# Performance work log

Measured on AMD Instinct MI355X. Metric: run time of the kernel, lower is better.

Reference implementation:

```python
import jax, jax.numpy as jnp
import numpy as np

B, T, N, F = 32, 64, 256, 64
TOP_K = 0.2  # ratio of dims to keep per batch element


def setup_inputs() -> dict:
    key = jax.random.key(0)
    ks = jax.random.split(key, 12)
    w = lambda k, shape: jax.random.normal(k, shape, jnp.float32) * 0.05
    z = lambda: jnp.zeros((F,), jnp.float32)
    return {
        "x": jax.random.normal(ks[0], (B, T, N, F), jnp.float32),
        "Wc1": w(ks[1], (3, F, F)), "bc1": z(),
        "Wc2": w(ks[2], (3, F, F)), "bc2": z(),
        "Wc3": w(ks[3], (3, F, F)), "bc3": z(),
        "Wq": w(ks[4], (F, F)), "bq": z(),
        "Wk": w(ks[5], (F, F)), "bk": z(),
        "Wv": w(ks[6], (F, F)), "bv": z(),
        "Wd": w(ks[7], (F, F)), "bd": z(),
        "Wp": w(ks[8], (F, F)), "bp": z(),
    }


def _conv1d(x, W, b, dil):
    # x: [BN, T, F], W: [3, F, F] (WIO), dilated same-padded conv over time
    y = jax.lax.conv_general_dilated(
        x, W, window_strides=(1,), padding="SAME", rhs_dilation=(dil,),
        dimension_numbers=("NWC", "WIO", "NWC"))
    return y + b


@jax.custom_vjp
def ste_round(x):
    return jnp.round(x)

def _ste_fwd(x):
    return jnp.round(x), None

def _ste_bwd(res, g):
    # activation='linear': grad = upstream * 1
    return (g,)

ste_round.defvjp(_ste_fwd, _ste_bwd)


def reference(x, Wc1, bc1, Wc2, bc2, Wc3, bc3, Wq, bq, Wk, bk, Wv, bv, Wd, bd, Wp, bp):
    Bx, Tx, Nx, Fx = x.shape
    # --- dilated conv block over time axis (per node) ---
    xt = jnp.transpose(x, (0, 2, 1, 3)).reshape(Bx * Nx, Tx, Fx)  # [BN,T,F]
    c = jax.nn.relu(_conv1d(xt, Wc1, bc1, 1) + _conv1d(xt, Wc2, bc2, 2)
                    + _conv1d(xt, Wc3, bc3, 3))
    xt = xt + c
    x = jnp.transpose(xt.reshape(Bx, Nx, Tx, Fx), (0, 2, 1, 3))  # [B,T,N,F]
    # --- GAT attention over nodes (faithful: diagonal einsum 'btnn,btnf->btnf') ---
    Q = x @ Wq + bq
    K = x @ Wk + bk
    V = x @ Wv + bv
    scores = jnp.einsum("btnf,btmf->btnm", Q, K) / jnp.sqrt(jnp.float32(Fx))
    A = jax.nn.softmax(scores, axis=-1)
    g = jnp.einsum("btnn,btnf->btnf", A, V)  # diag(A) * V, as in the TF source
    x = x + jax.nn.relu(g)
    # --- dense projection ---
    x = x @ Wd + bd
    # --- inf-norm normalize over last axis, rescale to [0,1] ---
    norm = jnp.max(jnp.abs(x), axis=-1, keepdims=True)
    x = x / norm
    x = 0.5 * (x + 1.0)
    # --- per-batch top-k threshold via full sort ---
    n = Tx * Nx * Fx
    k = int(round(TOP_K * n))  # top_k < 1 => ratio, statically resolved
    ranking = jnp.sort(x.reshape(Bx, -1), axis=-1)  # ascending
    mu = ranking[:, -k - 1].reshape(Bx, 1, 1, 1)
    x = jax.nn.sigmoid(x - mu)
    # --- straight-through binary mask + frozen linear predictor ---
    mask = ste_round(x)
    masked = x * mask
    pred_on_masked = masked @ Wp + bp
    return pred_on_masked, mask
```

## Files before the change

kernel.cpp:

```cpp
#include <hip/hip_runtime.h>
#include <math.h>

#define BB 32
#define TT 64
#define NNODES 256
#define FDIM 64
#define SLICE (NNODES*FDIM)
#define NTOT (BB*TT*NNODES*FDIM)
#define RANK0 838860u

typedef float v2f __attribute__((ext_vector_type(2)));
__device__ __forceinline__ v2f pkfma(v2f a, v2f b, v2f c) {
#if __has_builtin(__builtin_elementwise_fma)
  return __builtin_elementwise_fma(a, b, c);
#else
  v2f r; r.x = fmaf(a.x,b.x,c.x); r.y = fmaf(a.y,b.y,c.y); return r;
#endif
}

__global__ __launch_bounds__(256) void combine_w(
    const float* __restrict__ Wc1, const float* __restrict__ bc1,
    const float* __restrict__ Wc2, const float* __restrict__ bc2,
    const float* __restrict__ Wc3, const float* __restrict__ bc3,
    float* __restrict__ Wcomb, float* __restrict__ bcomb)
{
  const int FF2 = FDIM*FDIM;
  int gid = blockIdx.x*256 + threadIdx.x;
  if (gid < 7*FF2) {
    int j = gid / FF2, r = gid % FF2;
    float v;
    switch (j) {
      case 0: v = Wc3[r]; break;
      case 1: v = Wc2[r]; break;
      case 2: v = Wc1[r]; break;
      case 3: v = Wc1[FF2+r] + Wc2[FF2+r] + Wc3[FF2+r]; break;
      case 4: v = Wc1[2*FF2+r]; break;
      case 5: v = Wc2[2*FF2+r]; break;
      default: v = Wc3[2*FF2+r]; break;
    }
    Wcomb[gid] = v;
  }
  if (gid < FDIM) bcomb[gid] = bc1[gid] + bc2[gid] + bc3[gid];
}

__global__ __launch_bounds__(256) void combine_qk(
    const float* __restrict__ Wq, const float* __restrict__ bq,
    const float* __restrict__ Wk, const float* __restrict__ bk,
    float* __restrict__ Wqk, float* __restrict__ zb,
    float* __restrict__ wqbk, float* __restrict__ bqbk)
{
  int gid = blockIdx.x*256 + threadIdx.x;
  if (gid < 4096) {
    int i = gid >> 6, j = gid & 63;
    float a = 0.f;
    for (int o=0;o<64;o++) a = fmaf(Wq[i*64+o], Wk[j*64+o], a);
    Wqk[i*64+j] = a;
  } else if (gid < 4160) {
    int j = gid - 4096;
    float a = 0.f;
    for (int o=0;o<64;o++) a = fmaf(bq[o], Wk[j*64+o], a);
    zb[j] = a;
  } else if (gid < 4224) {
    int i = gid - 4160;
    float a = 0.f;
    for (int o=0;o<64;o++) a = fmaf(Wq[i*64+o], bk[o], a);
    wqbk[i] = a;
  } else if (gid == 4224) {
    float a = 0.f;
    for (int o=0;o<64;o++) a = fmaf(bq[o], bk[o], a);
    bqbk[0] = a;
  }
}

__global__ __launch_bounds__(256,4) void conv_kernel(
    const float* __restrict__ x, const float* __restrict__ Wcomb,
    const float* __restrict__ bcomb, float* __restrict__ x1)
{
  __shared__ float xs[64*72];
  const int bn = blockIdx.x; const int b = bn >> 8; const int n = bn & 255;
  const int tid = threadIdx.x;
#pragma unroll
  for (int k=0;k<18;k++) xs[k*256+tid] = 0.f;
  __syncthreads();
  const float* xbase = x + ((size_t)b*TT)*SLICE + n*FDIM;
#pragma unroll
  for (int it=0; it<4; it++) {
    int flat4 = it*256 + tid;
    int t = flat4 >> 4, f4 = (flat4 & 15) << 2;
    float4 v = *(const float4*)(xbase + (size_t)t*SLICE + f4);
    xs[(f4+0)*72 + t+4] = v.x;
    xs[(f4+1)*72 + t+4] = v.y;
    xs[(f4+2)*72 + t+4] = v.z;
    xs[(f4+3)*72 + t+4] = v.w;
  }
  __syncthreads();
  const int o = tid & 63;
  const int tb = (tid >> 6) << 4;
  float acc[16];
  const float bco = bcomb[o];
#pragma unroll
  for (int k=0;k<16;k++) acc[k] = bco;
  for (int i=0;i<FDIM;i++) {
    float xr[24];
#pragma unroll
    for (int q=0;q<6;q++) {
      float4 v = *(const float4*)&xs[i*72 + tb + q*4];
      xr[q*4+0]=v.x; xr[q*4+1]=v.y; xr[q*4+2]=v.z; xr[q*4+3]=v.w;
    }
#pragma unroll
    for (int j=0;j<7;j++) {
      float w = Wcomb[(j*FDIM+i)*FDIM + o];
#pragma unroll
      for (int k=0;k<16;k++) acc[k] = fmaf(xr[k+j+1], w, acc[k]);
    }
  }
  float* obase = x1 + ((size_t)b*TT)*SLICE + n*FDIM + o;
#pragma unroll
  for (int k=0;k<16;k++) {
    int t = tb + k;
    float c = acc[k];
    float outv = xs[o*72 + t+4] + (c > 0.f ? c : 0.f);
    obase[(size_t)t*SLICE] = outv;
  }
}

__global__ __launch_bounds__(256,2) void attn_kernel(
    const float* __restrict__ x1,
    const float* __restrict__ Wqk, const float* __restrict__ zb,
    const float* __restrict__ wqbk, const float* __restrict__ bqbk,
    const float* __restrict__ Wv, const float* __restrict__ bv,
    const float* __restrict__ Wd, const float* __restrict__ bd,
    float* __restrict__ vout)
{
  __shared__ float ks[NNODES*68];
  const int bt = blockIdx.x;
  const int tid = threadIdx.x;
  const float4* xb4 = (const float4*)(x1 + (size_t)bt*SLICE);
#pragma unroll
  for (int it=0; it<16; it++) {
    int flat4 = it*256 + tid;
    int n = flat4 >> 4, f4 = (flat4 & 15) << 2;
    *(float4*)&ks[n*68 + f4] = xb4[flat4];
  }
  __syncthreads();

  v2f zp[32];
  float d = bqbk[0];
  {
    float xr[64];
#pragma unroll
    for (int q=0;q<16;q++) {
      float4 v = *(const float4*)&ks[tid*68 + q*4];
      xr[q*4+0]=v.x; xr[q*4+1]=v.y; xr[q*4+2]=v.z; xr[q*4+3]=v.w;
    }
#pragma unroll
    for (int j=0;j<32;j++) { v2f t; t.x = zb[2*j]; t.y = zb[2*j+1]; zp[j] = t; }
    for (int i=0;i<64;i++) {
      v2f xv; xv.x = xr[i]; xv.y = xr[i];
      const float4* wr = (const float4*)(Wqk + i*64);
#pragma unroll
      for (int q=0;q<16;q++) {
        float4 w4 = wr[q];
        v2f wlo; wlo.x=w4.x; wlo.y=w4.y;
        v2f whi; whi.x=w4.z; whi.y=w4.w;
        zp[2*q]   = pkfma(xv, wlo, zp[2*q]);
        zp[2*q+1] = pkfma(xv, whi, zp[2*q+1]);
      }
      d = fmaf(xr[i], wqbk[i], d);
    }
  }

  float S0 = 0.f, S1 = 0.f, diag = 0.f;
  for (int m=0;m<NNODES;m+=2) {
    v2f a0={0.f,0.f}, a1={0.f,0.f}, b0={0.f,0.f}, b1={0.f,0.f};
#pragma unroll
    for (int q=0;q<16;q++) {
      float4 k0 = *(const float4*)&ks[m*68 + q*4];
      float4 k1 = *(const float4*)&ks[(m+1)*68 + q*4];
      v2f k0lo; k0lo.x=k0.x; k0lo.y=k0.y;
      v2f k0hi; k0hi.x=k0.z; k0hi.y=k0.w;
      v2f k1lo; k1lo.x=k1.x; k1lo.y=k1.y;
      v2f k1hi; k1hi.x=k1.z; k1hi.y=k1.w;
      a0 = pkfma(zp[2*q],   k0lo, a0);
      a1 = pkfma(zp[2*q+1], k0hi, a1);
      b0 = pkfma(zp[2*q],   k1lo, b0);
      b1 = pkfma(zp[2*q+1], k1hi, b1);
    }
    float s0 = (((a0.x+a0.y)+(a1.x+a1.y)) + d)*0.125f;
    float s1 = (((b0.x+b0.y)+(b1.x+b1.y)) + d)*0.125f;
    if (tid == m)   diag = s0;
    if (tid == m+1) diag = s1;
    S0 += __expf(s0);
    S1 += __expf(s1);
  }
  const float ann = __expf(diag) / (S0 + S1);

  float o1[64];
  {
    float xr[64];
#pragma unroll
    for (int q=0;q<16;q++) {
      float4 v = *(const float4*)&ks[tid*68 + q*4];
      xr[q*4+0]=v.x; xr[q*4+1]=v.y; xr[q*4+2]=v.z; xr[q*4+3]=v.w;
    }
    v2f vacc[32];
#pragma unroll
    for (int j=0;j<32;j++) { v2f t; t.x = bv[2*j]; t.y = bv[2*j+1]; vacc[j] = t; }
    for (int i=0;i<64;i++) {
      v2f xv; xv.x = xr[i]; xv.y = xr[i];
      const float4* wr = (const float4*)(Wv + i*64);
#pragma unroll
      for (int q=0;q<16;q++) {
        float4 w4 = wr[q];
        v2f wlo; wlo.x=w4.x; wlo.y=w4.y;
        v2f whi; whi.x=w4.z; whi.y=w4.w;
        vacc[2*q]   = pkfma(xv, wlo, vacc[2*q]);
        vacc[2*q+1] = pkfma(xv, whi, vacc[2*q+1]);
      }
    }
#pragma unroll
    for (int o=0;o<64;o++) {
      float g = ann * ((o & 1) ? vacc[o>>1].y : vacc[o>>1].x);
      o1[o] = xr[o] + (g > 0.f ? g : 0.f);
    }
  }
  float dd[64];
  {
    v2f dacc[32];
#pragma unroll
    for (int j=0;j<32;j++) { v2f t; t.x = bd[2*j]; t.y = bd[2*j+1]; dacc[j] = t; }
    for (int i=0;i<64;i++) {
      v2f xv; xv.x = o1[i]; xv.y = o1[i];
      const float4* wr = (const float4*)(Wd + i*64);
#pragma unroll
      for (int q=0;q<16;q++) {
        float4 w4 = wr[q];
        v2f wlo; wlo.x=w4.x; wlo.y=w4.y;
        v2f whi; whi.x=w4.z; whi.y=w4.w;
        dacc[2*q]   = pkfma(xv, wlo, dacc[2*q]);
        dacc[2*q+1] = pkfma(xv, whi, dacc[2*q+1]);
      }
    }
#pragma unroll
    for (int o=0;o<64;o++) dd[o] = (o & 1) ? dacc[o>>1].y : dacc[o>>1].x;
  }
  float nrm = 0.f;
#pragma unroll
  for (int o=0;o<64;o++) nrm = fmaxf(nrm, fabsf(dd[o]));
  __syncthreads();
#pragma unroll
  for (int q=0;q<16;q++) {
    float4 w;
    w.x = 0.5f*(dd[q*4+0]/nrm + 1.f);
    w.y = 0.5f*(dd[q*4+1]/nrm + 1.f);
    w.z = 0.5f*(dd[q*4+2]/nrm + 1.f);
    w.w = 0.5f*(dd[q*4+3]/nrm + 1.f);
    *(float4*)&ks[tid*68 + q*4] = w;
  }
  __syncthreads();
  float4* ob4 = (float4*)(vout + (size_t)bt*SLICE);
#pragma unroll
  for (int it=0;it<16;it++) {
    int flat4 = it*256 + tid;
    int n = flat4 >> 4, f4 = (flat4 & 15) << 2;
    ob4[flat4] = *(const float4*)&ks[n*68 + f4];
  }
}

template<int LEVEL>
__global__ __launch_bounds__(256) void hist_kernel(
    const float* __restrict__ v, unsigned* __restrict__ ghist,
    const unsigned* __restrict__ pfx)
{
  __shared__ unsigned h[4096];
  const int batch = blockIdx.x >> 5, chunk = blockIdx.x & 31;
  const int tid = threadIdx.x;
#pragma unroll
  for (int k=0;k<16;k++) h[k*256+tid] = 0u;
  __syncthreads();
  const unsigned p = pfx ? pfx[batch] : 0u;
  const float4* vb = (const float4*)(v + (size_t)batch*(TT*SLICE)) + chunk*8192 + tid;
  for (int k=0;k<32;k++) {
    float4 q = vb[k*256];
    float e[4] = {q.x,q.y,q.z,q.w};
#pragma unroll
    for (int j=0;j<4;j++) {
      unsigned u = __float_as_uint(e[j]);
      if (LEVEL==1) atomicAdd(&h[u>>20], 1u);
      else if ((u>>20)==p) atomicAdd(&h[(u>>8)&0xFFFu], 1u);
    }
  }
  __syncthreads();
  unsigned* gh = ghist + batch*4096;
#pragma unroll
  for (int k=0;k<16;k++) { unsigned c = h[k*256+tid]; if (c) atomicAdd(&gh[k*256+tid], c); }
}

__global__ __launch_bounds__(256) void hist8_kernel(
    const float* __restrict__ v, unsigned* __restrict__ ghist,
    const unsigned* __restrict__ pfx)
{
  __shared__ unsigned h[256];
  const int batch = blockIdx.x >> 5, chunk = blockIdx.x & 31;
  const int tid = threadIdx.x;
  h[tid] = 0u;
  __syncthreads();
  const unsigned p = pfx[batch];
  const float4* vb = (const float4*)(v + (size_t)batch*(TT*SLICE)) + chunk*8192 + tid;
  for (int k=0;k<32;k++) {
    float4 q = vb[k*256];
    float e[4] = {q.x,q.y,q.z,q.w};
#pragma unroll
    for (int j=0;j<4;j++) {
      unsigned u = __float_as_uint(e[j]);
      if ((u>>8)==p) atomicAdd(&h[u & 255u], 1u);
    }
  }
  __syncthreads();
  unsigned c = h[tid];
  if (c) atomicAdd(&ghist[batch*256+tid], c);
}

template<int PER>
__global__ __launch_bounds__(256) void find_kernel(
    const unsigned* __restrict__ hist,
    const unsigned* __restrict__ rank_in, const unsigned* __restrict__ pfx_in,
    int pfx_shift, unsigned* __restrict__ pfx_out, unsigned* __restrict__ rank_out,
    float* __restrict__ mu, int final_level)
{
  __shared__ unsigned csum[256];
  const int batch = blockIdx.x;
  const int tid = threadIdx.x;
  const unsigned* hb = hist + batch*(PER*256);
  unsigned loc[PER];
  unsigned s = 0;
#pragma unroll
  for (int q=0;q<PER;q++) { loc[q] = hb[tid*PER+q]; s += loc[q]; }
  csum[tid] = s;
  __syncthreads();
  for (int off=1; off<256; off<<=1) {
    unsigned vv = csum[tid];
    unsigned ad = (tid >= off) ? csum[tid-off] : 0u;
    __syncthreads();
    csum[tid] = vv + ad;
    __syncthreads();
  }
  const unsigned rank = rank_in ? rank_in[batch] : RANK0;
  const unsigned excl = csum[tid] - s;
  if (rank >= excl && rank < excl + s) {
    unsigned r = rank - excl;
    int bin = 0;
#pragma unroll
    for (int q=0;q<PER;q++) {
      if (r < loc[q]) { bin = tid*PER + q; break; }
      r -= loc[q];
    }
    unsigned pf = pfx_in ? pfx_in[batch] : 0u;
    unsigned np = (pf << pfx_shift) | (unsigned)bin;
    if (final_level) { mu[batch] = __uint_as_float(np); }
    else { pfx_out[batch] = np; rank_out[batch] = r; }
  }
}

__global__ __launch_bounds__(256,2) void final_kernel(
    const float* __restrict__ v, const float* __restrict__ mu,
    const float* __restrict__ Wp, const float* __restrict__ bp,
    float* __restrict__ pred, float* __restrict__ mask)
{
  __shared__ float sl[NNODES*68];
  const int bt = blockIdx.x;
  const int b = bt >> 6;
  const int tid = threadIdx.x;
  const float4* vb4 = (const float4*)(v + (size_t)bt*SLICE);
#pragma unroll
  for (int it=0; it<16; it++) {
    int flat4 = it*256 + tid;
    int n = flat4 >> 4, f4 = (flat4 & 15) << 2;
    *(float4*)&sl[n*68 + f4] = vb4[flat4];
  }
  __syncthreads();
  const float muv = mu[b];
  float srow[64];
#pragma unroll
  for (int q=0;q<16;q++) {
    float4 vv = *(const float4*)&sl[tid*68 + q*4];
    float e0 = 1.f/(1.f + expf(-(vv.x - muv)));
    float e1 = 1.f/(1.f + expf(-(vv.y - muv)));
    float e2 = 1.f/(1.f + expf(-(vv.z - muv)));
    float e3 = 1.f/(1.f + expf(-(vv.w - muv)));
    float m0 = rintf(e0), m1 = rintf(e1), m2 = rintf(e2), m3 = rintf(e3);
    srow[q*4+0] = e0*m0; srow[q*4+1] = e1*m1; srow[q*4+2] = e2*m2; srow[q*4+3] = e3*m3;
    float4 w; w.x=m0; w.y=m1; w.z=m2; w.w=m3;
    *(float4*)&sl[tid*68 + q*4] = w;
  }
  __syncthreads();
  float4* mb4 = (float4*)(mask + (size_t)bt*SLICE);
#pragma unroll
  for (int it=0; it<16; it++) {
    int flat4 = it*256 + tid;
    int n = flat4 >> 4, f4 = (flat4 & 15) << 2;
    mb4[flat4] = *(const float4*)&sl[n*68 + f4];
  }
  float acc[64];
#pragma unroll
  for (int o=0;o<64;o++) acc[o]=0.f;
  for (int i=0;i<64;i++) {
    float sv = srow[i];
#pragma unroll
    for (int o=0;o<64;o++) acc[o] = fmaf(sv, Wp[i*64+o], acc[o]);
  }
  __syncthreads();
#pragma unroll
  for (int q=0;q<16;q++) {
    float4 w;
    w.x = acc[q*4+0]+bp[q*4+0]; w.y = acc[q*4+1]+bp[q*4+1];
    w.z = acc[q*4+2]+bp[q*4+2]; w.w = acc[q*4+3]+bp[q*4+3];
    *(float4*)&sl[tid*68 + q*4] = w;
  }
  __syncthreads();
  float4* pb4 = (float4*)(pred + (size_t)bt*SLICE);
#pragma unroll
  for (int it=0; it<16; it++) {
    int flat4 = it*256 + tid;
    int n = flat4 >> 4, f4 = (flat4 & 15) << 2;
    pb4[flat4] = *(const float4*)&sl[n*68 + f4];
  }
}

extern "C" void kernel_launch(void* const* d_in, const int* in_sizes, int n_in,
                              void* d_out, int out_size, void* d_ws, size_t ws_size,
                              hipStream_t stream) {
  const float* x   = (const float*)d_in[0];
  const float* Wc1 = (const float*)d_in[1];  const float* bc1 = (const float*)d_in[2];
  const float* Wc2 = (const float*)d_in[3];  const float* bc2 = (const float*)d_in[4];
  const float* Wc3 = (const float*)d_in[5];  const float* bc3 = (const float*)d_in[6];
  const float* Wq  = (const float*)d_in[7];  const float* bq  = (const float*)d_in[8];
  const float* Wk  = (const float*)d_in[9];  const float* bk  = (const float*)d_in[10];
  const float* Wv  = (const float*)d_in[11]; const float* bv  = (const float*)d_in[12];
  const float* Wd  = (const float*)d_in[13]; const float* bd  = (const float*)d_in[14];
  const float* Wp  = (const float*)d_in[15]; const float* bp  = (const float*)d_in[16];

  float* pred = (float*)d_out;
  float* mask = pred + NTOT;

  unsigned* hist1 = (unsigned*)d_ws;
  unsigned* hist2 = hist1 + 32*4096;
  unsigned* hist3 = hist2 + 32*4096;
  unsigned* pfx1  = hist3 + 32*256;
  unsigned* rank1 = pfx1 + 32;
  unsigned* pfx2  = rank1 + 32;
  unsigned* rank2 = pfx2 + 32;
  float*    muv   = (float*)(rank2 + 32);
  float*    Wcomb = muv + 32;
  float*    bcomb = Wcomb + 7*64*64;
  float*    Wqk   = bcomb + 64;
  float*    zbv   = Wqk + 64*64;
  float*    wqbk  = zbv + 64;
  float*    bqbk  = wqbk + 64;

  hipMemsetAsync(d_ws, 0, (size_t)(32*4096*2 + 32*256)*sizeof(unsigned), stream);
  combine_w<<<112, 256, 0, stream>>>(Wc1,bc1,Wc2,bc2,Wc3,bc3,Wcomb,bcomb);
  combine_qk<<<17, 256, 0, stream>>>(Wq,bq,Wk,bk,Wqk,zbv,wqbk,bqbk);
  conv_kernel<<<BB*NNODES, 256, 0, stream>>>(x, Wcomb, bcomb, mask );
  attn_kernel<<<BB*TT, 256, 0, stream>>>(mask , Wqk,zbv,wqbk,bqbk, Wv,bv,Wd,bd, pred );
  hist_kernel<1><<<1024, 256, 0, stream>>>(pred, hist1, nullptr);
  find_kernel<16><<<32, 256, 0, stream>>>(hist1, nullptr, nullptr, 0, pfx1, rank1, nullptr, 0);
  hist_kernel<2><<<1024, 256, 0, stream>>>(pred, hist2, pfx1);
  find_kernel<16><<<32, 256, 0, stream>>>(hist2, rank1, pfx1, 12, pfx2, rank2, nullptr, 0);
  hist8_kernel<<<1024, 256, 0, stream>>>(pred, hist3, pfx2);
  find_kernel<1><<<32, 256, 0, stream>>>(hist3, rank2, pfx2, 8, nullptr, nullptr, muv, 1);
  final_kernel<<<BB*TT, 256, 0, stream>>>(pred , muv, Wp, bp, pred, mask);
}
```

Measured before the change: 1.196 ms.

## Register-tile the attention score pass and drop softmax-invariant bias terms

The attention kernel now stores each node's projected query (z = x·Wqk + zb) in shared memory and computes the score matrix as a register-tiled 4x8 outer-product block per thread, reading keys (x rows) straight from global/L2. Before, each thread swept all 256 key rows serially from LDS. The per-row constant term (x·Wq·bk + bq·bk) is removed because softmax is invariant to a per-row shift, which also removes the wqbk/bqbk precomputation. This should raise arithmetic intensity of the dominant N^2·F score pass, at the cost of more global loads of x and cross-lane shuffles to reduce the partial sums.

```diff
diff --git a/kernel.cpp b/kernel.cpp
--- a/kernel.cpp
+++ b/kernel.cpp
@@ -45,9 +45,8 @@
 
 __global__ __launch_bounds__(256) void combine_qk(
     const float* __restrict__ Wq, const float* __restrict__ bq,
-    const float* __restrict__ Wk, const float* __restrict__ bk,
-    float* __restrict__ Wqk, float* __restrict__ zb,
-    float* __restrict__ wqbk, float* __restrict__ bqbk)
+    const float* __restrict__ Wk,
+    float* __restrict__ Wqk, float* __restrict__ zb)
 {
   int gid = blockIdx.x*256 + threadIdx.x;
   if (gid < 4096) {
@@ -60,15 +59,6 @@
     float a = 0.f;
     for (int o=0;o<64;o++) a = fmaf(bq[o], Wk[j*64+o], a);
     zb[j] = a;
-  } else if (gid < 4224) {
-    int i = gid - 4160;
-    float a = 0.f;
-    for (int o=0;o<64;o++) a = fmaf(Wq[i*64+o], bk[o], a);
-    wqbk[i] = a;
-  } else if (gid == 4224) {
-    float a = 0.f;
-    for (int o=0;o<64;o++) a = fmaf(bq[o], bk[o], a);
-    bqbk[0] = a;
   }
 }
 
@@ -127,32 +117,26 @@
 __global__ __launch_bounds__(256,2) void attn_kernel(
     const float* __restrict__ x1,
     const float* __restrict__ Wqk, const float* __restrict__ zb,
-    const float* __restrict__ wqbk, const float* __restrict__ bqbk,
     const float* __restrict__ Wv, const float* __restrict__ bv,
     const float* __restrict__ Wd, const float* __restrict__ bd,
     float* __restrict__ vout)
 {
-  __shared__ float ks[NNODES*68];
+  __shared__ float zs[NNODES*68];
   const int bt = blockIdx.x;
   const int tid = threadIdx.x;
-  const float4* xb4 = (const float4*)(x1 + (size_t)bt*SLICE);
-#pragma unroll
-  for (int it=0; it<16; it++) {
-    int flat4 = it*256 + tid;
-    int n = flat4 >> 4, f4 = (flat4 & 15) << 2;
-    *(float4*)&ks[n*68 + f4] = xb4[flat4];
-  }
-  __syncthreads();
-
-  v2f zp[32];
-  float d = bqbk[0];
+  const int w = tid >> 6, l = tid & 63;
+  const int r = l & 15, g = l >> 4;
+  const float* xsl = x1 + (size_t)bt*SLICE;
+
   {
     float xr[64];
+    const float4* xrow = (const float4*)(xsl + tid*64);
 #pragma unroll
     for (int q=0;q<16;q++) {
-      float4 v = *(const float4*)&ks[tid*68 + q*4];
-      xr[q*4+0]=v.x; xr[q*4+1]=v.y; xr[q*4+2]=v.z; xr[q*4+3]=v.w;
-    }
+      float4 v = xrow[q];
+      xr[4*q]=v.x; xr[4*q+1]=v.y; xr[4*q+2]=v.z; xr[4*q+3]=v.w;
+    }
+    v2f zp[32];
 #pragma unroll
     for (int j=0;j<32;j++) { v2f t; t.x = zb[2*j]; t.y = zb[2*j+1]; zp[j] = t; }
     for (int i=0;i<64;i++) {
@@ -166,43 +150,83 @@
         zp[2*q]   = pkfma(xv, wlo, zp[2*q]);
         zp[2*q+1] = pkfma(xv, whi, zp[2*q+1]);
       }
-      d = fmaf(xr[i], wqbk[i], d);
-    }
-  }
-
-  float S0 = 0.f, S1 = 0.f, diag = 0.f;
-  for (int m=0;m<NNODES;m+=2) {
-    v2f a0={0.f,0.f}, a1={0.f,0.f}, b0={0.f,0.f}, b1={0.f,0.f};
+    }
 #pragma unroll
     for (int q=0;q<16;q++) {
-      float4 k0 = *(const float4*)&ks[m*68 + q*4];
-      float4 k1 = *(const float4*)&ks[(m+1)*68 + q*4];
-      v2f k0lo; k0lo.x=k0.x; k0lo.y=k0.y;
-      v2f k0hi; k0hi.x=k0.z; k0hi.y=k0.w;
-      v2f k1lo; k1lo.x=k1.x; k1lo.y=k1.y;
-      v2f k1hi; k1hi.x=k1.z; k1hi.y=k1.w;
-      a0 = pkfma(zp[2*q],   k0lo, a0);
-      a1 = pkfma(zp[2*q+1], k0hi, a1);
-      b0 = pkfma(zp[2*q],   k1lo, b0);
-      b1 = pkfma(zp[2*q+1], k1hi, b1);
-    }
-    float s0 = (((a0.x+a0.y)+(a1.x+a1.y)) + d)*0.125f;
-    float s1 = (((b0.x+b0.y)+(b1.x+b1.y)) + d)*0.125f;
-    if (tid == m)   diag = s0;
-    if (tid == m+1) diag = s1;
-    S0 += __expf(s0);
-    S1 += __expf(s1);
-  }
-  const float ann = __expf(diag) / (S0 + S1);
+      float4 t; t.x=zp[2*q].x; t.y=zp[2*q].y; t.z=zp[2*q+1].x; t.w=zp[2*q+1].y;
+      *(float4*)&zs[tid*68 + 4*q] = t;
+    }
+  }
+  __syncthreads();
+
+  const int zr0 = (64*w + r)*68;
+  const float* xqb = xsl + (64*g)*64;
+  float S[4] = {0.f,0.f,0.f,0.f};
+  for (int T=0; T<8; T++) {
+    v2f acc[4][8];
+    const float* xtb = xqb + (8*T)*64;
+#pragma unroll
+    for (int kc=0; kc<16; kc++) {
+      float4 zc[4];
+#pragma unroll
+      for (int j=0;j<4;j++) zc[j] = *(const float4*)&zs[zr0 + j*(16*68) + kc*4];
+      float4 xc[8];
+#pragma unroll
+      for (int i=0;i<8;i++) xc[i] = *(const float4*)(xtb + i*64 + kc*4);
+#pragma unroll
+      for (int j=0;j<4;j++) {
+        v2f zlo; zlo.x=zc[j].x; zlo.y=zc[j].y;
+        v2f zhi; zhi.x=zc[j].z; zhi.y=zc[j].w;
+#pragma unroll
+        for (int i=0;i<8;i++) {
+          v2f xlo; xlo.x=xc[i].x; xlo.y=xc[i].y;
+          v2f xhi; xhi.x=xc[i].z; xhi.y=xc[i].w;
+          if (kc == 0) acc[j][i] = zlo * xlo;
+          else         acc[j][i] = pkfma(zlo, xlo, acc[j][i]);
+          acc[j][i] = pkfma(zhi, xhi, acc[j][i]);
+        }
+      }
+    }
+#pragma unroll
+    for (int j=0;j<4;j++) {
+      float e = 0.f;
+#pragma unroll
+      for (int i=0;i<8;i++) {
+        float s = (acc[j][i].x + acc[j][i].y) * 0.125f;
+        e += __expf(s);
+      }
+      S[j] += e;
+    }
+  }
+#pragma unroll
+  for (int j=0;j<4;j++) {
+    S[j] += __shfl_xor(S[j], 16);
+    S[j] += __shfl_xor(S[j], 32);
+  }
+  const float Ss = (g==0) ? S[0] : (g==1) ? S[1] : (g==2) ? S[2] : S[3];
+
+  float xr[64];
+  {
+    const float4* xrow = (const float4*)(xsl + tid*64);
+#pragma unroll
+    for (int q=0;q<16;q++) {
+      float4 v = xrow[q];
+      xr[4*q]=v.x; xr[4*q+1]=v.y; xr[4*q+2]=v.z; xr[4*q+3]=v.w;
+    }
+  }
+  float diag = 0.f;
+#pragma unroll
+  for (int q=0;q<16;q++) {
+    float4 zv = *(const float4*)&zs[tid*68 + 4*q];
+    diag = fmaf(zv.x, xr[4*q],   diag);
+    diag = fmaf(zv.y, xr[4*q+1], diag);
+    diag = fmaf(zv.z, xr[4*q+2], diag);
+    diag = fmaf(zv.w, xr[4*q+3], diag);
+  }
+  const float ann = __expf(diag * 0.125f) / Ss;
 
   float o1[64];
   {
-    float xr[64];
-#pragma unroll
-    for (int q=0;q<16;q++) {
-      float4 v = *(const float4*)&ks[tid*68 + q*4];
-      xr[q*4+0]=v.x; xr[q*4+1]=v.y; xr[q*4+2]=v.z; xr[q*4+3]=v.w;
-    }
     v2f vacc[32];
 #pragma unroll
     for (int j=0;j<32;j++) { v2f t; t.x = bv[2*j]; t.y = bv[2*j+1]; vacc[j] = t; }
@@ -220,8 +244,8 @@
     }
 #pragma unroll
     for (int o=0;o<64;o++) {
-      float g = ann * ((o & 1) ? vacc[o>>1].y : vacc[o>>1].x);
-      o1[o] = xr[o] + (g > 0.f ? g : 0.f);
+      float gg = ann * ((o & 1) ? vacc[o>>1].y : vacc[o>>1].x);
+      o1[o] = xr[o] + (gg > 0.f ? gg : 0.f);
     }
   }
   float dd[64];
@@ -250,12 +274,12 @@
   __syncthreads();
 #pragma unroll
   for (int q=0;q<16;q++) {
-    float4 w;
-    w.x = 0.5f*(dd[q*4+0]/nrm + 1.f);
-    w.y = 0.5f*(dd[q*4+1]/nrm + 1.f);
-    w.z = 0.5f*(dd[q*4+2]/nrm + 1.f);
-    w.w = 0.5f*(dd[q*4+3]/nrm + 1.f);
-    *(float4*)&ks[tid*68 + q*4] = w;
+    float4 wv4;
+    wv4.x = 0.5f*(dd[q*4+0]/nrm + 1.f);
+    wv4.y = 0.5f*(dd[q*4+1]/nrm + 1.f);
+    wv4.z = 0.5f*(dd[q*4+2]/nrm + 1.f);
+    wv4.w = 0.5f*(dd[q*4+3]/nrm + 1.f);
+    *(float4*)&zs[tid*68 + q*4] = wv4;
   }
   __syncthreads();
   float4* ob4 = (float4*)(vout + (size_t)bt*SLICE);
@@ -263,7 +287,7 @@
   for (int it=0;it<16;it++) {
     int flat4 = it*256 + tid;
     int n = flat4 >> 4, f4 = (flat4 & 15) << 2;
-    ob4[flat4] = *(const float4*)&ks[n*68 + f4];
+    ob4[flat4] = *(const float4*)&zs[n*68 + f4];
   }
 }
 
@@ -435,7 +459,7 @@
   const float* Wc2 = (const float*)d_in[3];  const float* bc2 = (const float*)d_in[4];
   const float* Wc3 = (const float*)d_in[5];  const float* bc3 = (const float*)d_in[6];
   const float* Wq  = (const float*)d_in[7];  const float* bq  = (const float*)d_in[8];
-  const float* Wk  = (const float*)d_in[9];  const float* bk  = (const float*)d_in[10];
+  const float* Wk  = (const float*)d_in[9];
   const float* Wv  = (const float*)d_in[11]; const float* bv  = (const float*)d_in[12];
   const float* Wd  = (const float*)d_in[13]; const float* bd  = (const float*)d_in[14];
   const float* Wp  = (const float*)d_in[15]; const float* bp  = (const float*)d_in[16];
@@ -455,14 +479,12 @@
   float*    bcomb = Wcomb + 7*64*64;
   float*    Wqk   = bcomb + 64;
   float*    zbv   = Wqk + 64*64;
-  float*    wqbk  = zbv + 64;
-  float*    bqbk  = wqbk + 64;
 
   hipMemsetAsync(d_ws, 0, (size_t)(32*4096*2 + 32*256)*sizeof(unsigned), stream);
   combine_w<<<112, 256, 0, stream>>>(Wc1,bc1,Wc2,bc2,Wc3,bc3,Wcomb,bcomb);
-  combine_qk<<<17, 256, 0, stream>>>(Wq,bq,Wk,bk,Wqk,zbv,wqbk,bqbk);
+  combine_qk<<<17, 256, 0, stream>>>(Wq,bq,Wk,Wqk,zbv);
   conv_kernel<<<BB*NNODES, 256, 0, stream>>>(x, Wcomb, bcomb, mask );
-  attn_kernel<<<BB*TT, 256, 0, stream>>>(mask , Wqk,zbv,wqbk,bqbk, Wv,bv,Wd,bd, pred );
+  attn_kernel<<<BB*TT, 256, 0, stream>>>(mask , Wqk,zbv, Wv,bv,Wd,bd, pred );
   hist_kernel<1><<<1024, 256, 0, stream>>>(pred, hist1, nullptr);
   find_kernel<16><<<32, 256, 0, stream>>>(hist1, nullptr, nullptr, 0, pfx1, rank1, nullptr, 0);
   hist_kernel<2><<<1024, 256, 0, stream>>>(pred, hist2, pfx1);
```

Result: slower. 1.983 ms (+65.8%).
